# Kernel tuning notes

Measured on AMD Instinct MI355X. Metric: run time of the kernel, lower is better.

## Reference

```python
import jax, jax.numpy as jnp
import numpy as np

BS, N, DEG = 2, 16384, 16
NE = N * DEG          # 262144 edges
D = 128               # node/edge feature dim
S = 4                 # number of completed blocks
EPS = 1e-6


def mlp(x, W1, b1, W2, b2):
    # MLP(in, hidden=128, out, act=SiLU, layer_norm=False)
    return jax.nn.silu(x @ W1 + b1) @ W2 + b2


def rms_norm(x, w):
    return x * jax.lax.rsqrt(jnp.mean(x * x, axis=-1, keepdims=True) + EPS) * w


def setup_inputs() -> dict:
    key = jax.random.key(0)
    ks = jax.random.split(key, 14)
    f32 = jnp.float32
    sc = 0.05
    return {
        "V": jax.random.normal(ks[0], (BS, N, D), f32),
        "E": jax.random.normal(ks[1], (BS, NE, D), f32),
        "blocks": jax.random.normal(ks[2], (S, BS, N, D), f32),
        "We1": jax.random.normal(ks[3], (3 * D, D), f32) * sc,
        "be1": jnp.zeros((D,), f32),
        "We2": jax.random.normal(ks[4], (D, D), f32) * sc,
        "be2": jnp.zeros((D,), f32),
        "Wn1": jax.random.normal(ks[5], (2 * D, D), f32) * sc,
        "bn1": jnp.zeros((D,), f32),
        "Wn2": jax.random.normal(ks[6], (D, D), f32) * sc,
        "bn2": jnp.zeros((D,), f32),
        "w_attn": jax.random.normal(ks[7], (D,), f32) * sc,
        "rms_w": jnp.ones((D,), f32),
        "edges": jax.random.randint(ks[8], (BS, NE, 2), 0, N, jnp.int32),
    }


def reference(V, E, blocks, We1, be1, We2, be2, Wn1, bn1, Wn2, bn2,
              w_attn, rms_w, edges):
    # ---- GNN layer: edge gather -> edge MLP -> scatter_mean -> node MLP ----
    senders = jnp.take_along_axis(V, edges[..., 0][:, :, None], axis=1)    # [b,E,D]
    receivers = jnp.take_along_axis(V, edges[..., 1][:, :, None], axis=1)  # [b,E,D]
    edge_inpt = jnp.concatenate([senders, receivers, E], axis=-1)          # [b,E,3D]
    edge_emb = mlp(edge_inpt, We1, be1, We2, be2)                          # [b,E,D]
    e0, e1 = jnp.split(edge_emb, 2, axis=-1)                               # [b,E,D/2] each

    def seg_mean(vals, idx):
        s = jax.ops.segment_sum(vals, idx, num_segments=N)
        c = jax.ops.segment_sum(jnp.ones(idx.shape, vals.dtype), idx,
                                num_segments=N)
        return s / jnp.maximum(c, 1.0)[:, None]

    m0 = jax.vmap(seg_mean)(e0, edges[..., 0])   # [b,N,D/2]
    m1 = jax.vmap(seg_mean)(e1, edges[..., 1])   # [b,N,D/2]
    node_inpt = jnp.concatenate([V, m0, m1], axis=-1)                      # [b,N,2D]
    node_emb = mlp(node_inpt, Wn1, bn1, Wn2, bn2)                          # [b,N,D]

    # ---- block_attn_res: depth-wise attention over stacked blocks ----
    Vs = jnp.concatenate([blocks, node_emb[None]], axis=0)                 # [S+1,b,N,D]
    K = rms_norm(Vs, rms_w)
    logits = jnp.einsum('d,sbnd->sbn', w_attn, K)
    alpha = jax.nn.softmax(logits, axis=0)
    h = jnp.einsum('sbn,sbnd->bnd', alpha, Vs)                             # [b,N,D]
    return h
```

## Files before the change

kernel.cpp:

```cpp
#include <hip/hip_runtime.h>
#include <hip/hip_bf16.h>

#define D 128
#define NNODES 16384
#define NEDGES 262144
#define NBATCH 2
#define TE 64

typedef __attribute__((ext_vector_type(8))) short bf16x8;
typedef __attribute__((ext_vector_type(4))) float f32x4;

__device__ __forceinline__ unsigned short f2bf(float f) {
    unsigned int u = __float_as_uint(f);
    unsigned int r = (u + 0x7fffu + ((u >> 16) & 1u)) >> 16;
    return (unsigned short)r;
}

__device__ __forceinline__ unsigned int pk2bf(float lo, float hi) {
    return (unsigned int)f2bf(lo) | ((unsigned int)f2bf(hi) << 16);
}

__device__ __forceinline__ float bf2f(unsigned short u) {
    return __uint_as_float(((unsigned int)u) << 16);
}

__global__ __launch_bounds__(256)
void prep_weights(const float* __restrict__ We1, const float* __restrict__ We2,
                  const float* __restrict__ Wn1, const float* __restrict__ Wn2,
                  unsigned short* __restrict__ w)
{
    int id = blockIdx.x * 256 + threadIdx.x;
    if (id < 16384) {
        int e = id & 7, l = (id >> 3) & 63, nblk = (id >> 9) & 7, ks = id >> 12;
        int k = 256 + ks * 32 + ((l >> 4) & 3) * 8 + e;
        int col = nblk * 16 + (l & 15);
        w[id] = f2bf(We1[k * 128 + col]);
    } else if (id < 32768) {
        int i2 = id - 16384;
        int e = i2 & 7, l = (i2 >> 3) & 63, nblk = (i2 >> 9) & 7, ks = i2 >> 12;
        int k = ks * 32 + ((l >> 4) & 3) * 8 + e;
        int col = nblk * 16 + (l & 15);
        w[id] = f2bf(We2[k * 128 + col]);
    } else if (id < 65536) {
        int i3 = id - 32768;
        int j = i3 >> 7, k = i3 & 127;
        int row = (j < 128) ? k : (128 + k);
        w[id] = f2bf(We1[row * 128 + (j & 127)]);
    } else if (id < 98304) {
        int i4 = id - 65536;
        int n = i4 >> 8, k = i4 & 255;
        w[id] = f2bf(Wn1[k * 128 + n]);
    } else {
        int i5 = id - 98304;
        int n = i5 >> 7, k = i5 & 127;
        w[id] = f2bf(Wn2[k * 128 + n]);
    }
}

__global__ __launch_bounds__(256)
void partial_kernel(const float* __restrict__ V, const unsigned short* __restrict__ wp,
                    unsigned short* __restrict__ P)
{
    __shared__ unsigned short smem[64 * 136];
    const int t = threadIdx.x, lane = t & 63, wave = t >> 6;
    const int l15 = lane & 15, l4 = lane >> 4;
    const long long r0 = (long long)blockIdx.x * 64;

    for (int i = t; i < 64 * 32; i += 256) {
        int c4 = i & 31, r = i >> 5;
        float4 v = *(const float4*)(V + (r0 + r) * 128 + c4 * 4);
        uint2 p; p.x = pk2bf(v.x, v.y); p.y = pk2bf(v.z, v.w);
        *(uint2*)(&smem[r * 136 + c4 * 4]) = p;
    }
    __syncthreads();

    const int j0 = wave * 64;
    f32x4 acc[4][4] = {};
    const unsigned short* bb0 = wp + (j0 + l15) * 128 + l4 * 8;
    #pragma unroll
    for (int ks = 0; ks < 4; ++ks) {
        bf16x8 bb[4];
        #pragma unroll
        for (int n = 0; n < 4; ++n)
            bb[n] = *(const bf16x8*)(bb0 + n * 16 * 128 + ks * 32);
        #pragma unroll
        for (int mq = 0; mq < 4; ++mq) {
            bf16x8 a = *(const bf16x8*)(&smem[(mq * 16 + l15) * 136 + l4 * 8 + ks * 32]);
            #pragma unroll
            for (int n = 0; n < 4; ++n)
                acc[mq][n] = __builtin_amdgcn_mfma_f32_16x16x32_bf16(a, bb[n], acc[mq][n], 0, 0, 0);
        }
    }
    #pragma unroll
    for (int mq = 0; mq < 4; ++mq) {
        #pragma unroll
        for (int n = 0; n < 4; ++n) {
            #pragma unroll
            for (int i = 0; i < 4; ++i) {
                int row = mq * 16 + l4 * 4 + i;
                int col = j0 + n * 16 + l15;
                P[(r0 + row) * 256 + col] = f2bf(acc[mq][n][i]);
            }
        }
    }
}

__global__ __launch_bounds__(256)
void edge_kernel(const float* __restrict__ E, const int* __restrict__ edges,
                 const unsigned short* __restrict__ P,
                 const unsigned short* __restrict__ w1ef, const float* __restrict__ be1,
                 const unsigned short* __restrict__ w2f, const float* __restrict__ be2,
                 float* __restrict__ m0sum, float* __restrict__ m1sum,
                 float* __restrict__ c0, float* __restrict__ c1)
{
    __shared__ unsigned short smem[TE * 136];
    __shared__ int eidx[TE][2];

    const int t    = threadIdx.x;
    const int lane = t & 63;
    const int wave = t >> 6;
    const int wr   = wave >> 1;
    const int wc   = wave & 1;
    const int l15  = lane & 15;
    const int l4   = lane >> 4;

    const long long eflat0 = (long long)blockIdx.x * TE;
    const int b  = (int)(eflat0 / NEDGES);

    if (t < TE * 2) {
        eidx[t >> 1][t & 1] = edges[(eflat0 + (t >> 1)) * 2 + (t & 1)];
    }
    for (int i = t; i < TE * 32; i += 256) {
        int c4 = i & 31, e = i >> 5;
        float4 v = *(const float4*)(E + (eflat0 + e) * D + c4 * 4);
        uint2 p; p.x = pk2bf(v.x, v.y); p.y = pk2bf(v.z, v.w);
        *(uint2*)(&smem[e * 136 + c4 * 4]) = p;
    }
    __syncthreads();

    f32x4 acc[2][4] = {};
    {
        const unsigned short* arow = &smem[(wr * 32 + l15) * 136 + l4 * 8];
        #pragma unroll
        for (int ks = 0; ks < 4; ++ks) {
            bf16x8 a0 = *(const bf16x8*)(arow + ks * 32);
            bf16x8 a1 = *(const bf16x8*)(arow + 16 * 136 + ks * 32);
            #pragma unroll
            for (int n = 0; n < 4; ++n) {
                bf16x8 bb = *(const bf16x8*)(w1ef + (((ks * 8 + wc * 4 + n) * 64 + lane) << 3));
                acc[0][n] = __builtin_amdgcn_mfma_f32_16x16x32_bf16(a0, bb, acc[0][n], 0, 0, 0);
                acc[1][n] = __builtin_amdgcn_mfma_f32_16x16x32_bf16(a1, bb, acc[1][n], 0, 0, 0);
            }
        }
    }
    __syncthreads();

    const long long pb0 = (long long)b * NNODES;
    #pragma unroll
    for (int n = 0; n < 4; ++n) {
        int col = wc * 64 + n * 16 + l15;
        float bias = be1[col];
        #pragma unroll
        for (int m = 0; m < 2; ++m) {
            #pragma unroll
            for (int i = 0; i < 4; ++i) {
                int row = wr * 32 + m * 16 + l4 * 4 + i;
                long long ps = (pb0 + eidx[row][0]) * 256 + col;
                long long pr = (pb0 + eidx[row][1]) * 256 + 128 + col;
                float a = acc[m][n][i] + bias + bf2f(P[ps]) + bf2f(P[pr]);
                smem[row * 136 + col] = f2bf(a / (1.f + __expf(-a)));
            }
        }
    }
    __syncthreads();

    f32x4 acc2[2][4] = {};
    {
        const unsigned short* hrow = &smem[(wr * 32 + l15) * 136 + l4 * 8];
        #pragma unroll
        for (int ks = 0; ks < 4; ++ks) {
            bf16x8 a0 = *(const bf16x8*)(hrow + ks * 32);
            bf16x8 a1 = *(const bf16x8*)(hrow + 16 * 136 + ks * 32);
            #pragma unroll
            for (int n = 0; n < 4; ++n) {
                bf16x8 bb = *(const bf16x8*)(w2f + (((ks * 8 + wc * 4 + n) * 64 + lane) << 3));
                acc2[0][n] = __builtin_amdgcn_mfma_f32_16x16x32_bf16(a0, bb, acc2[0][n], 0, 0, 0);
                acc2[1][n] = __builtin_amdgcn_mfma_f32_16x16x32_bf16(a1, bb, acc2[1][n], 0, 0, 0);
            }
        }
    }

    float* dst_arr = wc ? m1sum : m0sum;
    const long long nb0 = (long long)b * NNODES;
    #pragma unroll
    for (int n = 0; n < 4; ++n) {
        int colh = n * 16 + l15;
        float bias = be2[wc * 64 + colh];
        #pragma unroll
        for (int m = 0; m < 2; ++m) {
            #pragma unroll
            for (int i = 0; i < 4; ++i) {
                int erow = wr * 32 + m * 16 + l4 * 4 + i;
                int node = eidx[erow][wc];
                atomicAdd(dst_arr + (nb0 + node) * 64 + colh,
                          acc2[m][n][i] + bias);
            }
        }
    }
    if (t < TE)          atomicAdd(&c0[nb0 + eidx[t][0]], 1.f);
    else if (t < 2 * TE) atomicAdd(&c1[nb0 + eidx[t - TE][1]], 1.f);
}

__global__ __launch_bounds__(256)
void node_kernel(const float* __restrict__ V,
                 const float* __restrict__ m0sum, const float* __restrict__ m1sum,
                 const float* __restrict__ c0, const float* __restrict__ c1,
                 const unsigned short* __restrict__ wn1t, const float* __restrict__ bn1,
                 const unsigned short* __restrict__ wn2t, const float* __restrict__ bn2,
                 float* __restrict__ node_emb)
{
    __shared__ unsigned short smem[TE * 264];

    const int t    = threadIdx.x;
    const int lane = t & 63;
    const int wave = t >> 6;
    const int wr   = wave >> 1;
    const int wc   = wave & 1;
    const int l15  = lane & 15;
    const int l4   = lane >> 4;

    const long long nflat0 = (long long)blockIdx.x * TE;

    for (int i = t; i < TE * 64; i += 256) {
        int c4 = i & 63;
        int n  = i >> 6;
        long long node = nflat0 + n;
        float4 v; int off;
        if (c4 < 32) {
            v = *(const float4*)(V + node * 128 + c4 * 4);
            off = c4 * 4;
        } else if (c4 < 48) {
            v = *(const float4*)(m0sum + node * 64 + (c4 - 32) * 4);
            float inv = 1.f / fmaxf(c0[node], 1.f);
            v.x *= inv; v.y *= inv; v.z *= inv; v.w *= inv;
            off = 128 + (c4 - 32) * 4;
        } else {
            v = *(const float4*)(m1sum + node * 64 + (c4 - 48) * 4);
            float inv = 1.f / fmaxf(c1[node], 1.f);
            v.x *= inv; v.y *= inv; v.z *= inv; v.w *= inv;
            off = 192 + (c4 - 48) * 4;
        }
        uint2 p;
        p.x = pk2bf(v.x, v.y);
        p.y = pk2bf(v.z, v.w);
        *(uint2*)(&smem[n * 264 + c4 * 4]) = p;
    }
    __syncthreads();

    f32x4 acc[2][4] = {};
    {
        const unsigned short* arow = &smem[(wr * 32 + l15) * 264 + l4 * 8];
        const unsigned short* bb0  = wn1t + (wc * 64 + l15) * 256 + l4 * 8;
        for (int ks = 0; ks < 8; ++ks) {
            bf16x8 a0 = *(const bf16x8*)(arow + ks * 32);
            bf16x8 a1 = *(const bf16x8*)(arow + 16 * 264 + ks * 32);
            #pragma unroll
            for (int n = 0; n < 4; ++n) {
                bf16x8 bb = *(const bf16x8*)(bb0 + n * 16 * 256 + ks * 32);
                acc[0][n] = __builtin_amdgcn_mfma_f32_16x16x32_bf16(a0, bb, acc[0][n], 0, 0, 0);
                acc[1][n] = __builtin_amdgcn_mfma_f32_16x16x32_bf16(a1, bb, acc[1][n], 0, 0, 0);
            }
        }
    }
    __syncthreads();

    #pragma unroll
    for (int n = 0; n < 4; ++n) {
        int col = wc * 64 + n * 16 + l15;
        float bias = bn1[col];
        #pragma unroll
        for (int m = 0; m < 2; ++m) {
            #pragma unroll
            for (int i = 0; i < 4; ++i) {
                int row = wr * 32 + m * 16 + l4 * 4 + i;
                float a = acc[m][n][i] + bias;
                smem[row * 136 + col] = f2bf(a / (1.f + __expf(-a)));
            }
        }
    }
    __syncthreads();

    f32x4 acc2[2][4] = {};
    {
        const unsigned short* hrow = &smem[(wr * 32 + l15) * 136 + l4 * 8];
        const unsigned short* bb0  = wn2t + (wc * 64 + l15) * 128 + l4 * 8;
        #pragma unroll
        for (int ks = 0; ks < 4; ++ks) {
            bf16x8 a0 = *(const bf16x8*)(hrow + ks * 32);
            bf16x8 a1 = *(const bf16x8*)(hrow + 16 * 136 + ks * 32);
            #pragma unroll
            for (int n = 0; n < 4; ++n) {
                bf16x8 bb = *(const bf16x8*)(bb0 + n * 16 * 128 + ks * 32);
                acc2[0][n] = __builtin_amdgcn_mfma_f32_16x16x32_bf16(a0, bb, acc2[0][n], 0, 0, 0);
                acc2[1][n] = __builtin_amdgcn_mfma_f32_16x16x32_bf16(a1, bb, acc2[1][n], 0, 0, 0);
            }
        }
    }

    #pragma unroll
    for (int n = 0; n < 4; ++n) {
        int col = wc * 64 + n * 16 + l15;
        float bias = bn2[col];
        #pragma unroll
        for (int m = 0; m < 2; ++m) {
            #pragma unroll
            for (int i = 0; i < 4; ++i) {
                long long row = nflat0 + wr * 32 + m * 16 + l4 * 4 + i;
                node_emb[row * 128 + col] = acc2[m][n][i] + bias;
            }
        }
    }
}

__global__ __launch_bounds__(256)
void attn_kernel(const float* __restrict__ blocks, const float* __restrict__ node_emb,
                 const float* __restrict__ w_attn, const float* __restrict__ rms_w,
                 float* __restrict__ out)
{
    const int t    = threadIdx.x;
    const int wave = t >> 6;
    const int lane = t & 63;
    const long long node = (long long)blockIdx.x * 4 + wave;
    const int d0 = lane * 2;

    float2 wa = *(const float2*)(w_attn + d0);
    float2 rw = *(const float2*)(rms_w + d0);

    float xs[5][2];
    float lg[5];
    #pragma unroll
    for (int s = 0; s < 5; ++s) {
        const float* src = (s < 4)
            ? (blocks + ((long long)s * NBATCH * NNODES + node) * 128)
            : (node_emb + node * 128);
        float2 x = *(const float2*)(src + d0);
        xs[s][0] = x.x; xs[s][1] = x.y;
        float ss = x.x * x.x + x.y * x.y;
        float wv = wa.x * rw.x * x.x + wa.y * rw.y * x.y;
        #pragma unroll
        for (int m = 1; m < 64; m <<= 1) {
            ss += __shfl_xor(ss, m);
            wv += __shfl_xor(wv, m);
        }
        lg[s] = wv * rsqrtf(ss * (1.f / 128.f) + 1e-6f);
    }

    float mx = lg[0];
    #pragma unroll
    for (int s = 1; s < 5; ++s) mx = fmaxf(mx, lg[s]);
    float ex[5], sum = 0.f;
    #pragma unroll
    for (int s = 0; s < 5; ++s) { ex[s] = __expf(lg[s] - mx); sum += ex[s]; }
    float inv = 1.f / sum;

    float h0 = 0.f, h1 = 0.f;
    #pragma unroll
    for (int s = 0; s < 5; ++s) {
        float a = ex[s] * inv;
        h0 = fmaf(a, xs[s][0], h0);
        h1 = fmaf(a, xs[s][1], h1);
    }
    *(float2*)(out + node * 128 + d0) = make_float2(h0, h1);
}

extern "C" void kernel_launch(void* const* d_in, const int* in_sizes, int n_in,
                              void* d_out, int out_size, void* d_ws, size_t ws_size,
                              hipStream_t stream)
{
    const float* V      = (const float*)d_in[0];
    const float* E      = (const float*)d_in[1];
    const float* blocks = (const float*)d_in[2];
    const float* We1    = (const float*)d_in[3];
    const float* be1    = (const float*)d_in[4];
    const float* We2    = (const float*)d_in[5];
    const float* be2    = (const float*)d_in[6];
    const float* Wn1    = (const float*)d_in[7];
    const float* bn1    = (const float*)d_in[8];
    const float* Wn2    = (const float*)d_in[9];
    const float* bn2    = (const float*)d_in[10];
    const float* w_attn = (const float*)d_in[11];
    const float* rms_w  = (const float*)d_in[12];
    const int*   edges  = (const int*)d_in[13];
    float* out = (float*)d_out;

    float* ws = (float*)d_ws;
    float* m0sum    = ws;
    float* m1sum    = m0sum + 2097152;
    float* c0       = m1sum + 2097152;
    float* c1       = c0 + 32768;
    float* node_emb = c1 + 32768;
    unsigned short* wbf = (unsigned short*)(node_emb + 4194304);
    unsigned short* w1ef = wbf;
    unsigned short* w2f  = wbf + 16384;
    unsigned short* wp   = wbf + 32768;
    unsigned short* wn1t = wbf + 65536;
    unsigned short* wn2t = wbf + 98304;
    unsigned short* P    = wbf + 114688;

    (void)hipMemsetAsync(d_ws, 0, (size_t)(2097152 * 2 + 32768 * 2) * sizeof(float), stream);

    prep_weights<<<448, 256, 0, stream>>>(We1, We2, Wn1, Wn2, wbf);

    partial_kernel<<<(NBATCH * NNODES) / 64, 256, 0, stream>>>(V, wp, P);

    edge_kernel<<<(NBATCH * NEDGES) / TE, 256, 0, stream>>>(
        E, edges, P, w1ef, be1, w2f, be2, m0sum, m1sum, c0, c1);

    node_kernel<<<(NBATCH * NNODES) / TE, 256, 0, stream>>>(
        V, m0sum, m1sum, c0, c1, wn1t, bn1, wn2t, bn2, node_emb);

    attn_kernel<<<(NBATCH * NNODES) / 4, 256, 0, stream>>>(
        blocks, node_emb, w_attn, rms_w, out);
}
```

Before: 383.9 us.

## Make edge kernel persistent with register prefetch of next edge tile

The edge kernel now runs a fixed grid of 2048 blocks, each looping over 4 edge tiles instead of one block per tile. The next tile's E rows and edge indices are loaded into registers while the current tile computes, and are written to shared memory at the end of the iteration. Separate E and hidden buffers let the first barrier be dropped. Node indices are cached in registers. The aim is to hide global load latency and cut launch and barrier overhead, at the cost of more registers and possibly lower occupancy.

```diff
diff --git a/kernel.cpp b/kernel.cpp
--- a/kernel.cpp
+++ b/kernel.cpp
@@ -6,6 +6,8 @@
 #define NEDGES 262144
 #define NBATCH 2
 #define TE 64
+#define EGRID 2048
+#define NT 4
 
 typedef __attribute__((ext_vector_type(8))) short bf16x8;
 typedef __attribute__((ext_vector_type(4))) float f32x4;
@@ -113,7 +115,8 @@
                  float* __restrict__ m0sum, float* __restrict__ m1sum,
                  float* __restrict__ c0, float* __restrict__ c1)
 {
-    __shared__ unsigned short smem[TE * 136];
+    __shared__ unsigned short Ebuf[TE * 136];
+    __shared__ unsigned short Hbuf[TE * 136];
     __shared__ int eidx[TE][2];
 
     const int t    = threadIdx.x;
@@ -123,92 +126,138 @@
     const int wc   = wave & 1;
     const int l15  = lane & 15;
     const int l4   = lane >> 4;
-
-    const long long eflat0 = (long long)blockIdx.x * TE;
-    const int b  = (int)(eflat0 / NEDGES);
-
-    if (t < TE * 2) {
-        eidx[t >> 1][t & 1] = edges[(eflat0 + (t >> 1)) * 2 + (t & 1)];
-    }
-    for (int i = t; i < TE * 32; i += 256) {
-        int c4 = i & 31, e = i >> 5;
-        float4 v = *(const float4*)(E + (eflat0 + e) * D + c4 * 4);
-        uint2 p; p.x = pk2bf(v.x, v.y); p.y = pk2bf(v.z, v.w);
-        *(uint2*)(&smem[e * 136 + c4 * 4]) = p;
+    const int sc4  = t & 31;
+    const int se0  = t >> 5;
+
+    float4 pre[8];
+    int preidx = 0;
+
+    long long tile = blockIdx.x;
+
+    {
+        const long long ef0 = tile * TE;
+        #pragma unroll
+        for (int j = 0; j < 8; ++j)
+            pre[j] = *(const float4*)(E + (ef0 + se0 + j * 8) * D + sc4 * 4);
+        if (t < TE * 2) preidx = edges[(ef0 + (t >> 1)) * 2 + (t & 1)];
+        #pragma unroll
+        for (int j = 0; j < 8; ++j) {
+            uint2 p; p.x = pk2bf(pre[j].x, pre[j].y); p.y = pk2bf(pre[j].z, pre[j].w);
+            *(uint2*)(&Ebuf[(se0 + j * 8) * 136 + sc4 * 4]) = p;
+        }
+        if (t < TE * 2) eidx[t >> 1][t & 1] = preidx;
     }
     __syncthreads();
 
-    f32x4 acc[2][4] = {};
-    {
-        const unsigned short* arow = &smem[(wr * 32 + l15) * 136 + l4 * 8];
-        #pragma unroll
-        for (int ks = 0; ks < 4; ++ks) {
-            bf16x8 a0 = *(const bf16x8*)(arow + ks * 32);
-            bf16x8 a1 = *(const bf16x8*)(arow + 16 * 136 + ks * 32);
-            #pragma unroll
-            for (int n = 0; n < 4; ++n) {
-                bf16x8 bb = *(const bf16x8*)(w1ef + (((ks * 8 + wc * 4 + n) * 64 + lane) << 3));
-                acc[0][n] = __builtin_amdgcn_mfma_f32_16x16x32_bf16(a0, bb, acc[0][n], 0, 0, 0);
-                acc[1][n] = __builtin_amdgcn_mfma_f32_16x16x32_bf16(a1, bb, acc[1][n], 0, 0, 0);
-            }
-        }
-    }
-    __syncthreads();
-
-    const long long pb0 = (long long)b * NNODES;
-    #pragma unroll
-    for (int n = 0; n < 4; ++n) {
-        int col = wc * 64 + n * 16 + l15;
-        float bias = be1[col];
+    for (int it = 0; it < NT; ++it) {
+        const bool have_next = (it + 1 < NT);
+        const long long tile_next = tile + EGRID;
+
+        if (have_next) {
+            const long long ef1 = tile_next * TE;
+            #pragma unroll
+            for (int j = 0; j < 8; ++j)
+                pre[j] = *(const float4*)(E + (ef1 + se0 + j * 8) * D + sc4 * 4);
+            if (t < TE * 2) preidx = edges[(ef1 + (t >> 1)) * 2 + (t & 1)];
+        }
+
+        const long long eflat0 = tile * TE;
+        const int b = (int)(eflat0 / NEDGES);
+        const long long nb0 = (long long)b * NNODES;
+
+        if (t < TE)          atomicAdd(&c0[nb0 + eidx[t][0]], 1.f);
+        else if (t < 2 * TE) atomicAdd(&c1[nb0 + eidx[t - TE][1]], 1.f);
+
+        f32x4 acc[2][4] = {};
+        {
+            const unsigned short* arow = &Ebuf[(wr * 32 + l15) * 136 + l4 * 8];
+            #pragma unroll
+            for (int ks = 0; ks < 4; ++ks) {
+                bf16x8 a0 = *(const bf16x8*)(arow + ks * 32);
+                bf16x8 a1 = *(const bf16x8*)(arow + 16 * 136 + ks * 32);
+                #pragma unroll
+                for (int n = 0; n < 4; ++n) {
+                    bf16x8 bb = *(const bf16x8*)(w1ef + (((ks * 8 + wc * 4 + n) * 64 + lane) << 3));
+                    acc[0][n] = __builtin_amdgcn_mfma_f32_16x16x32_bf16(a0, bb, acc[0][n], 0, 0, 0);
+                    acc[1][n] = __builtin_amdgcn_mfma_f32_16x16x32_bf16(a1, bb, acc[1][n], 0, 0, 0);
+                }
+            }
+        }
+
+        int nd0[2][4], nd1[2][4];
         #pragma unroll
         for (int m = 0; m < 2; ++m) {
             #pragma unroll
             for (int i = 0; i < 4; ++i) {
                 int row = wr * 32 + m * 16 + l4 * 4 + i;
-                long long ps = (pb0 + eidx[row][0]) * 256 + col;
-                long long pr = (pb0 + eidx[row][1]) * 256 + 128 + col;
-                float a = acc[m][n][i] + bias + bf2f(P[ps]) + bf2f(P[pr]);
-                smem[row * 136 + col] = f2bf(a / (1.f + __expf(-a)));
-            }
-        }
-    }
-    __syncthreads();
-
-    f32x4 acc2[2][4] = {};
-    {
-        const unsigned short* hrow = &smem[(wr * 32 + l15) * 136 + l4 * 8];
-        #pragma unroll
-        for (int ks = 0; ks < 4; ++ks) {
-            bf16x8 a0 = *(const bf16x8*)(hrow + ks * 32);
-            bf16x8 a1 = *(const bf16x8*)(hrow + 16 * 136 + ks * 32);
+                nd0[m][i] = eidx[row][0];
+                nd1[m][i] = eidx[row][1];
+            }
+        }
+
+        #pragma unroll
+        for (int n = 0; n < 4; ++n) {
+            int col = wc * 64 + n * 16 + l15;
+            float bias = be1[col];
+            #pragma unroll
+            for (int m = 0; m < 2; ++m) {
+                #pragma unroll
+                for (int i = 0; i < 4; ++i) {
+                    int row = wr * 32 + m * 16 + l4 * 4 + i;
+                    float a = acc[m][n][i] + bias
+                            + bf2f(P[(nb0 + nd0[m][i]) * 256 + col])
+                            + bf2f(P[(nb0 + nd1[m][i]) * 256 + 128 + col]);
+                    Hbuf[row * 136 + col] = f2bf(a / (1.f + __expf(-a)));
+                }
+            }
+        }
+        __syncthreads();
+
+        f32x4 acc2[2][4] = {};
+        {
+            const unsigned short* hrow = &Hbuf[(wr * 32 + l15) * 136 + l4 * 8];
+            #pragma unroll
+            for (int ks = 0; ks < 4; ++ks) {
+                bf16x8 a0 = *(const bf16x8*)(hrow + ks * 32);
+                bf16x8 a1 = *(const bf16x8*)(hrow + 16 * 136 + ks * 32);
+                #pragma unroll
+                for (int n = 0; n < 4; ++n) {
+                    bf16x8 bb = *(const bf16x8*)(w2f + (((ks * 8 + wc * 4 + n) * 64 + lane) << 3));
+                    acc2[0][n] = __builtin_amdgcn_mfma_f32_16x16x32_bf16(a0, bb, acc2[0][n], 0, 0, 0);
+                    acc2[1][n] = __builtin_amdgcn_mfma_f32_16x16x32_bf16(a1, bb, acc2[1][n], 0, 0, 0);
+                }
+            }
+        }
+
+        {
+            float* dst_arr = wc ? m1sum : m0sum;
             #pragma unroll
             for (int n = 0; n < 4; ++n) {
-                bf16x8 bb = *(const bf16x8*)(w2f + (((ks * 8 + wc * 4 + n) * 64 + lane) << 3));
-                acc2[0][n] = __builtin_amdgcn_mfma_f32_16x16x32_bf16(a0, bb, acc2[0][n], 0, 0, 0);
-                acc2[1][n] = __builtin_amdgcn_mfma_f32_16x16x32_bf16(a1, bb, acc2[1][n], 0, 0, 0);
-            }
-        }
-    }
-
-    float* dst_arr = wc ? m1sum : m0sum;
-    const long long nb0 = (long long)b * NNODES;
-    #pragma unroll
-    for (int n = 0; n < 4; ++n) {
-        int colh = n * 16 + l15;
-        float bias = be2[wc * 64 + colh];
-        #pragma unroll
-        for (int m = 0; m < 2; ++m) {
-            #pragma unroll
-            for (int i = 0; i < 4; ++i) {
-                int erow = wr * 32 + m * 16 + l4 * 4 + i;
-                int node = eidx[erow][wc];
-                atomicAdd(dst_arr + (nb0 + node) * 64 + colh,
-                          acc2[m][n][i] + bias);
-            }
-        }
-    }
-    if (t < TE)          atomicAdd(&c0[nb0 + eidx[t][0]], 1.f);
-    else if (t < 2 * TE) atomicAdd(&c1[nb0 + eidx[t - TE][1]], 1.f);
+                int colh = n * 16 + l15;
+                float bias = be2[wc * 64 + colh];
+                #pragma unroll
+                for (int m = 0; m < 2; ++m) {
+                    #pragma unroll
+                    for (int i = 0; i < 4; ++i) {
+                        int node = wc ? nd1[m][i] : nd0[m][i];
+                        atomicAdd(dst_arr + (nb0 + node) * 64 + colh,
+                                  acc2[m][n][i] + bias);
+                    }
+                }
+            }
+        }
+
+        if (have_next) {
+            #pragma unroll
+            for (int j = 0; j < 8; ++j) {
+                uint2 p; p.x = pk2bf(pre[j].x, pre[j].y); p.y = pk2bf(pre[j].z, pre[j].w);
+                *(uint2*)(&Ebuf[(se0 + j * 8) * 136 + sc4 * 4]) = p;
+            }
+            if (t < TE * 2) eidx[t >> 1][t & 1] = preidx;
+        }
+        __syncthreads();
+        tile = tile_next;
+    }
 }
 
 __global__ __launch_bounds__(256)
@@ -413,7 +462,7 @@
 
     partial_kernel<<<(NBATCH * NNODES) / 64, 256, 0, stream>>>(V, wp, P);
 
-    edge_kernel<<<(NBATCH * NEDGES) / TE, 256, 0, stream>>>(
+    edge_kernel<<<EGRID, 256, 0, stream>>>(
         E, edges, P, w1ef, be1, w2f, be2, m0sum, m1sum, c0, c1);
 
     node_kernel<<<(NBATCH * NNODES) / TE, 256, 0, stream>>>(
```

New measurement: 505.8 us. +31.8%, slower.
